# Kernel tuning notes

Hardware: AMD Instinct MI355X
Metric: run time of the kernel (lower is better)

## Reference

```python
import jax, jax.numpy as jnp
import numpy as np

B, S, D = 4, 4096, 256


def setup_inputs() -> dict:
    key = jax.random.key(0)
    k1, k2, k3, k4, k5 = jax.random.split(key, 5)
    query = jax.random.normal(k1, (B, S, D), dtype=jnp.float32)
    key_t = jax.random.normal(k2, (B, S, D), dtype=jnp.float32)
    value = jax.random.normal(k3, (B, S, D), dtype=jnp.float32)
    # nn.Linear(dim_model, dim_model): weight [D, D] (out, in), bias [D]
    bound = 1.0 / np.sqrt(D)
    Wq = jax.random.uniform(k4, (D, D), dtype=jnp.float32, minval=-bound, maxval=bound)
    bq = jax.random.uniform(k5, (D,), dtype=jnp.float32, minval=-bound, maxval=bound)
    return {"query": query, "key": key_t, "value": value, "Wq": Wq, "bq": bq}


def reference(query, key, value, Wq, bq):
    # Faithful to source: self.q is applied to ALL THREE inputs (source bug).
    q = jnp.einsum('bsd,od->bso', query, Wq) + bq  # [B,S,D]
    k = jnp.einsum('bsd,od->bso', key, Wq) + bq
    v = jnp.einsum('bsd,od->bso', value, Wq) + bq
    scale = jnp.sqrt(jnp.asarray(q.shape[-1], q.dtype))
    scores = jnp.einsum('bqd,bkd->bqk', q, k) / scale  # [B,S,S]
    attn = jax.nn.softmax(scores, axis=-1)
    return jnp.einsum('bqk,bkd->bqd', attn, v)  # [B,S,D]
```

## Files before the change

kernel.cpp:

```cpp
#include <hip/hip_runtime.h>


typedef __attribute__((ext_vector_type(4)))  float    f32x4;
typedef __attribute__((ext_vector_type(16))) float    f32x16;
typedef __attribute__((ext_vector_type(8)))  short    s16x8;
typedef __attribute__((ext_vector_type(2)))  unsigned u32x2;

#define AS_GLB const __attribute__((address_space(1))) unsigned
#define AS_LDS __attribute__((address_space(3))) unsigned

static constexpr float CEXP = 0.09016844f;
static constexpr float CM   = -32.0f * 0.09016844f;

static constexpr size_t QBF_OFF = 0;
static constexpr size_t KBF_OFF = 8ull  << 20;
static constexpr size_t VTB_OFF = 16ull << 20;
static constexpr size_t OT_OFF  = 24ull << 20;
static constexpr size_t LS_OFF  = 56ull << 20;

__device__ __forceinline__ unsigned bf16_rne(float f) {
  union { float f; unsigned u; } v; v.f = f;
  return (v.u + 0x7FFFu + ((v.u >> 16) & 1u)) >> 16;
}
__device__ __forceinline__ unsigned pkbf16(float a, float b) {
  return bf16_rne(a) | (bf16_rne(b) << 16);
}

__global__ __launch_bounds__(256, 2) void proj_kernel(
    const float* __restrict__ Xq, const float* __restrict__ Xk,
    const float* __restrict__ Xv, const float* __restrict__ Wq,
    const float* __restrict__ bq, char* __restrict__ ws)
{
  __shared__ char plds[32768];
  const int tid = threadIdx.x;
  const int lane = tid & 63, w = tid >> 6;
  const int wr = w >> 1, wc = w & 1;
  const int l15 = lane & 15, l4 = (lane >> 4) & 3;

  const int mt = blockIdx.x;
  const int tensor = mt >> 7;
  const int r0 = (mt & 127) << 7;
  const int n0 = blockIdx.y << 7;
  const float* A = (tensor == 0) ? Xq : (tensor == 1 ? Xk : Xv);

  f32x4 acc[4][4];
#pragma unroll
  for (int i = 0; i < 4; ++i)
#pragma unroll
    for (int j = 0; j < 4; ++j) { acc[i][j][0]=0.f; acc[i][j][1]=0.f; acc[i][j][2]=0.f; acc[i][j][3]=0.f; }

  for (int kt = 0; kt < 4; ++kt) {
    const int k0 = kt << 6;
#pragma unroll
    for (int j = 0; j < 8; ++j) {
      int c = j * 256 + tid;
      int row = c >> 4, col4 = c & 15;
      f32x4 av = *(const f32x4*)(A + (size_t)(r0 + row) * 256 + k0 + col4 * 4);
      u32x2 pa; pa[0] = pkbf16(av[0], av[1]); pa[1] = pkbf16(av[2], av[3]);
      int off = row * 128 + ((col4 * 8) ^ ((row & 7) << 4));
      *(u32x2*)(plds + off) = pa;
      f32x4 wv = *(const f32x4*)(Wq + (size_t)(n0 + row) * 256 + k0 + col4 * 4);
      u32x2 pw; pw[0] = pkbf16(wv[0], wv[1]); pw[1] = pkbf16(wv[2], wv[3]);
      *(u32x2*)(plds + 16384 + off) = pw;
    }
    __syncthreads();
#pragma unroll
    for (int ks = 0; ks < 2; ++ks) {
      s16x8 af[4], wf[4];
#pragma unroll
      for (int mi = 0; mi < 4; ++mi) {
        int row = wr * 64 + mi * 16 + l15;
        af[mi] = *(const s16x8*)(plds + row * 128 + ((ks * 64 + l4 * 16) ^ ((row & 7) << 4)));
      }
#pragma unroll
      for (int ni = 0; ni < 4; ++ni) {
        int row = wc * 64 + ni * 16 + l15;
        wf[ni] = *(const s16x8*)(plds + 16384 + row * 128 + ((ks * 64 + l4 * 16) ^ ((row & 7) << 4)));
      }
      if (tensor == 1) {
#pragma unroll
        for (int mi = 0; mi < 4; ++mi)
#pragma unroll
          for (int ni = 0; ni < 4; ++ni)
            acc[mi][ni] = __builtin_amdgcn_mfma_f32_16x16x32_bf16(wf[ni], af[mi], acc[mi][ni], 0, 0, 0);
      } else {
#pragma unroll
        for (int mi = 0; mi < 4; ++mi)
#pragma unroll
          for (int ni = 0; ni < 4; ++ni)
            acc[mi][ni] = __builtin_amdgcn_mfma_f32_16x16x32_bf16(af[mi], wf[ni], acc[mi][ni], 0, 0, 0);
      }
    }
    __syncthreads();
  }

  if (tensor == 0) {
    unsigned short* Qb = (unsigned short*)(ws + QBF_OFF);
#pragma unroll
    for (int ni = 0; ni < 4; ++ni) {
      int gn = n0 + wc * 64 + ni * 16 + l15;
      float bias = bq[gn];
#pragma unroll
      for (int mi = 0; mi < 4; ++mi) {
        int mrow = r0 + wr * 64 + mi * 16 + l4 * 4;
#pragma unroll
        for (int j = 0; j < 4; ++j)
          Qb[(size_t)(mrow + j) * 256 + gn] = (unsigned short)bf16_rne(acc[mi][ni][j] + bias);
      }
    }
  } else if (tensor == 1) {
    char* Kf = ws + KBF_OFF;
#pragma unroll
    for (int ni = 0; ni < 4; ++ni) {
      int dbase = n0 + wc * 64 + ni * 16 + l4 * 4;
      f32x4 bv = *(const f32x4*)(bq + dbase);
#pragma unroll
      for (int mi = 0; mi < 4; ++mi) {
        int s = r0 + wr * 64 + mi * 16 + l15;
        int b2 = s >> 12, sl = s & 31, kb = (s & 4095) >> 5;
        size_t chunk = (((size_t)b2 * 128 + kb) * 32 + (dbase >> 3)) * 32 + sl;
        u32x2 pv;
        pv[0] = pkbf16(acc[mi][ni][0] + bv[0], acc[mi][ni][1] + bv[1]);
        pv[1] = pkbf16(acc[mi][ni][2] + bv[2], acc[mi][ni][3] + bv[3]);
        *(u32x2*)(Kf + chunk * 16 + (dbase & 7) * 2) = pv;
      }
    }
  } else {
    char* Vf = ws + VTB_OFF;
#pragma unroll
    for (int ni = 0; ni < 4; ++ni) {
      int gn = n0 + wc * 64 + ni * 16 + l15;
      float bias = bq[gn];
#pragma unroll
      for (int mi = 0; mi < 4; ++mi) {
        int s = r0 + wr * 64 + mi * 16 + l4 * 4;
        int b2 = s >> 12, kb = (s & 4095) >> 5, sl = s & 31;
        size_t chunk = ((((size_t)b2 * 128 + kb) * 4 + (sl >> 3)) * 8 + (gn >> 5)) * 32 + (gn & 31);
        u32x2 pv;
        pv[0] = pkbf16(acc[mi][ni][0] + bias, acc[mi][ni][1] + bias);
        pv[1] = pkbf16(acc[mi][ni][2] + bias, acc[mi][ni][3] + bias);
        *(u32x2*)(Vf + chunk * 16 + (sl & 7) * 2) = pv;
      }
    }
  }
}

__global__ __launch_bounds__(256, 2) void flash_kernel(char* __restrict__ ws)
{
  __shared__ char lds[65536];
  const int tid = threadIdx.x;
  const int lane = tid & 63, w = tid >> 6;
  const int l31 = lane & 31, h = lane >> 5;

  const int bid  = blockIdx.x;
  const int sp   = bid & 3;
  const int b    = (bid >> 2) & 3;
  const int qblk = bid >> 4;
  const int q0w  = qblk * 128 + w * 32;
  const int kb0  = sp * 32;

  const char* Kfb = ws + KBF_OFF + (size_t)b * (2u << 20);
  const char* Vfb = ws + VTB_OFF + (size_t)b * (2u << 20);

  s16x8 qf[16];
  {
    const char* qrow = ws + QBF_OFF + (size_t)((b << 12) + q0w + l31) * 512 + h * 16;
#pragma unroll
    for (int i = 0; i < 16; ++i) qf[i] = *(const s16x8*)(qrow + i * 32);
  }
#pragma unroll
  for (int i = 0; i < 16; ++i) asm volatile("" :: "v"(qf[i]));

  f32x16 O[8];
#pragma unroll
  for (int t8 = 0; t8 < 8; ++t8)
#pragma unroll
    for (int r = 0; r < 16; ++r) O[t8][r] = 0.f;

  float l_run = 0.f;

  auto STAGE = [&](int buf, int t) {
    const char* ksrc = Kfb + (size_t)(kb0 + t) * 16384;
    const char* vsrc = Vfb + (size_t)(kb0 + t) * 16384;
#pragma unroll
    for (int i = 0; i < 4; ++i) {
      unsigned c = (unsigned)(w * 4 + i) << 10;
      __builtin_amdgcn_global_load_lds((AS_GLB*)(ksrc + c + (unsigned)lane * 16),
          (AS_LDS*)(lds + buf * 32768 + c), 16, 0, 0);
      __builtin_amdgcn_global_load_lds((AS_GLB*)(vsrc + c + (unsigned)lane * 16),
          (AS_LDS*)(lds + buf * 32768 + 16384 + c), 16, 0, 0);
    }
  };

  auto COMPUTE = [&](int buf) {
    const char* kb = lds + buf * 32768;
    const char* vb = kb + 16384;
    f32x16 pe, po;
#pragma unroll
    for (int r = 0; r < 16; ++r) { pe[r] = 0.f; po[r] = 0.f; }
    __builtin_amdgcn_s_setprio(1);
#pragma unroll
    for (int i = 0; i < 16; i += 2) {
      s16x8 kf0 = *(const s16x8*)(kb + (2 * i + h) * 512 + l31 * 16);
      pe = __builtin_amdgcn_mfma_f32_32x32x16_bf16(kf0, qf[i], pe, 0, 0, 0);
      s16x8 kf1 = *(const s16x8*)(kb + (2 * (i + 1) + h) * 512 + l31 * 16);
      po = __builtin_amdgcn_mfma_f32_32x32x16_bf16(kf1, qf[i + 1], po, 0, 0, 0);
    }
    __builtin_amdgcn_s_setprio(0);
    float p[16];
#pragma unroll
    for (int r = 0; r < 16; ++r)
      p[r] = __builtin_exp2f(__builtin_fmaf(pe[r] + po[r], CEXP, CM));
    float s0 = (p[0] + p[1]) + (p[2] + p[3]);
    float s1 = (p[4] + p[5]) + (p[6] + p[7]);
    float s2 = (p[8] + p[9]) + (p[10] + p[11]);
    float s3 = (p[12] + p[13]) + (p[14] + p[15]);
    l_run += (s0 + s1) + (s2 + s3);
    unsigned a0, a1, b0, b1, c0, c1, d0, d1;
    asm("v_cvt_pk_bf16_f32 %0, %1, %2" : "=v"(a0) : "v"(p[0]),  "v"(p[1]));
    asm("v_cvt_pk_bf16_f32 %0, %1, %2" : "=v"(a1) : "v"(p[2]),  "v"(p[3]));
    asm("v_cvt_pk_bf16_f32 %0, %1, %2" : "=v"(b0) : "v"(p[4]),  "v"(p[5]));
    asm("v_cvt_pk_bf16_f32 %0, %1, %2" : "=v"(b1) : "v"(p[6]),  "v"(p[7]));
    asm("v_cvt_pk_bf16_f32 %0, %1, %2" : "=v"(c0) : "v"(p[8]),  "v"(p[9]));
    asm("v_cvt_pk_bf16_f32 %0, %1, %2" : "=v"(c1) : "v"(p[10]), "v"(p[11]));
    asm("v_cvt_pk_bf16_f32 %0, %1, %2" : "=v"(d0) : "v"(p[12]), "v"(p[13]));
    asm("v_cvt_pk_bf16_f32 %0, %1, %2" : "=v"(d1) : "v"(p[14]), "v"(p[15]));
    asm("v_permlane32_swap_b32 %0, %1" : "+v"(a0), "+v"(b0));
    asm("v_permlane32_swap_b32 %0, %1" : "+v"(a1), "+v"(b1));
    asm("v_permlane32_swap_b32 %0, %1" : "+v"(c0), "+v"(d0));
    asm("v_permlane32_swap_b32 %0, %1" : "+v"(c1), "+v"(d1));
    union { s16x8 v; unsigned u[4]; } pa0, pa1;
    pa0.u[0] = a0; pa0.u[1] = a1; pa0.u[2] = b0; pa0.u[3] = b1;
    pa1.u[0] = c0; pa1.u[1] = c1; pa1.u[2] = d0; pa1.u[3] = d1;
    __builtin_amdgcn_s_setprio(1);
#pragma unroll
    for (int t8 = 0; t8 < 8; ++t8) {
      s16x8 v0 = *(const s16x8*)(vb + ((h * 8 + t8) << 9) + l31 * 16);
      O[t8] = __builtin_amdgcn_mfma_f32_32x32x16_bf16(pa0.v, v0, O[t8], 0, 0, 0);
      s16x8 v1 = *(const s16x8*)(vb + (((2 + h) * 8 + t8) << 9) + l31 * 16);
      O[t8] = __builtin_amdgcn_mfma_f32_32x32x16_bf16(pa1.v, v1, O[t8], 0, 0, 0);
    }
    __builtin_amdgcn_s_setprio(0);
  };

  STAGE(0, 0);
  for (int t = 0; t < 31; ++t) {
    STAGE((t + 1) & 1, t + 1);
    asm volatile("s_waitcnt vmcnt(8)" ::: "memory");
    __builtin_amdgcn_s_barrier();
    __builtin_amdgcn_sched_barrier(0);
    COMPUTE(t & 1);
    __builtin_amdgcn_s_barrier();
    __builtin_amdgcn_sched_barrier(0);
  }
  asm volatile("s_waitcnt vmcnt(0)" ::: "memory");
  __builtin_amdgcn_s_barrier();
  __builtin_amdgcn_sched_barrier(0);
  COMPUTE(1);

  l_run += __shfl_xor(l_run, 32, 64);

  unsigned short* OTb = (unsigned short*)(ws + OT_OFF) +
                        (((size_t)(sp * 4 + b) << 12) << 8);
#pragma unroll
  for (int t8 = 0; t8 < 8; ++t8) {
    int d = t8 * 32 + l31;
#pragma unroll
    for (int r = 0; r < 16; ++r) {
      int q = q0w + (r & 3) + 8 * (r >> 2) + 4 * h;
      OTb[(size_t)q * 256 + d] = (unsigned short)bf16_rne(O[t8][r]);
    }
  }
  if (lane < 32) {
    int idx = ((sp * 4 + b) << 12) + q0w + l31;
    ((float*)(ws + LS_OFF))[idx] = l_run;
  }
}

__global__ __launch_bounds__(256) void merge_kernel(const char* __restrict__ ws,
                                                    float* __restrict__ out)
{
  const int t = threadIdx.x;
  const int b = blockIdx.x;
  const int s0 = blockIdx.y << 4;
  const int soff = t >> 7, dd = (t & 127) * 2;
  const unsigned short* OTb = (const unsigned short*)(ws + OT_OFF);
  const float* Ls = (const float*)(ws + LS_OFF);
  for (int si = 0; si < 8; ++si) {
    int s = s0 + si * 2 + soff;
    float L = 0.f;
#pragma unroll
    for (int sp = 0; sp < 4; ++sp) L += Ls[((sp * 4 + b) << 12) + s];
    float rL = 1.0f / L;
    float a0 = 0.f, a1 = 0.f;
#pragma unroll
    for (int sp = 0; sp < 4; ++sp) {
      unsigned uv = *(const unsigned*)(OTb + ((((size_t)(sp * 4 + b) << 12) + s) << 8) + dd);
      union { unsigned u; float f; } lo, hi;
      lo.u = uv << 16; hi.u = uv & 0xFFFF0000u;
      a0 += lo.f; a1 += hi.f;
    }
    float2 o; o.x = a0 * rL; o.y = a1 * rL;
    *(float2*)(out + (((size_t)(b << 12) + s) << 8) + dd) = o;
  }
}

extern "C" void kernel_launch(void* const* d_in, const int* in_sizes, int n_in,
                              void* d_out, int out_size, void* d_ws, size_t ws_size,
                              hipStream_t stream) {
  const float* q  = (const float*)d_in[0];
  const float* k  = (const float*)d_in[1];
  const float* v  = (const float*)d_in[2];
  const float* Wq = (const float*)d_in[3];
  const float* bq = (const float*)d_in[4];
  char* ws = (char*)d_ws;
  float* out = (float*)d_out;
  hipLaunchKernelGGL(proj_kernel, dim3(384, 2), dim3(256), 0, stream, q, k, v, Wq, bq, ws);
  hipLaunchKernelGGL(flash_kernel, dim3(512), dim3(256), 0, stream, ws);
  hipLaunchKernelGGL(merge_kernel, dim3(4, 256), dim3(256), 0, stream, ws, out);
}
```

Measured before the change: 112.3 us.

## Software-pipeline QK and PV across iterations with split K/V staging

Restructures the attention loop so the PV matmul of the previous tile is issued after the QK matmul of the current tile, letting the exp/convert work of one tile overlap the MFMA work of another. K and V now use separate double buffers with separate staging, and V is loaded one iteration later than K. The two interleaved QK accumulators become a single one, which lengthens the dependent MFMA chain. The probabilities are carried across iterations in registers, which raises register pressure.

New measurement: 110.7 us. No clear change (-1.4%).

```diff
diff --git a/kernel.cpp b/kernel.cpp
--- a/kernel.cpp
+++ b/kernel.cpp
@@ -178,39 +178,65 @@
     for (int r = 0; r < 16; ++r) O[t8][r] = 0.f;
 
   float l_run = 0.f;
-
-  auto STAGE = [&](int buf, int t) {
+  s16x8 paP0, paP1;
+
+  auto STAGE_K = [&](int buf, int t) {
     const char* ksrc = Kfb + (size_t)(kb0 + t) * 16384;
-    const char* vsrc = Vfb + (size_t)(kb0 + t) * 16384;
 #pragma unroll
     for (int i = 0; i < 4; ++i) {
       unsigned c = (unsigned)(w * 4 + i) << 10;
       __builtin_amdgcn_global_load_lds((AS_GLB*)(ksrc + c + (unsigned)lane * 16),
-          (AS_LDS*)(lds + buf * 32768 + c), 16, 0, 0);
+          (AS_LDS*)(lds + buf * 16384 + c), 16, 0, 0);
+    }
+  };
+  auto STAGE_V = [&](int buf, int t) {
+    const char* vsrc = Vfb + (size_t)(kb0 + t) * 16384;
+#pragma unroll
+    for (int i = 0; i < 4; ++i) {
+      unsigned c = (unsigned)(w * 4 + i) << 10;
       __builtin_amdgcn_global_load_lds((AS_GLB*)(vsrc + c + (unsigned)lane * 16),
-          (AS_LDS*)(lds + buf * 32768 + 16384 + c), 16, 0, 0);
+          (AS_LDS*)(lds + 32768 + buf * 16384 + c), 16, 0, 0);
     }
   };
-
-  auto COMPUTE = [&](int buf) {
-    const char* kb = lds + buf * 32768;
-    const char* vb = kb + 16384;
-    f32x16 pe, po;
-#pragma unroll
-    for (int r = 0; r < 16; ++r) { pe[r] = 0.f; po[r] = 0.f; }
+  auto PV = [&](const char* vb, s16x8 a0, s16x8 a1) {
     __builtin_amdgcn_s_setprio(1);
 #pragma unroll
-    for (int i = 0; i < 16; i += 2) {
-      s16x8 kf0 = *(const s16x8*)(kb + (2 * i + h) * 512 + l31 * 16);
-      pe = __builtin_amdgcn_mfma_f32_32x32x16_bf16(kf0, qf[i], pe, 0, 0, 0);
-      s16x8 kf1 = *(const s16x8*)(kb + (2 * (i + 1) + h) * 512 + l31 * 16);
-      po = __builtin_amdgcn_mfma_f32_32x32x16_bf16(kf1, qf[i + 1], po, 0, 0, 0);
+    for (int t8 = 0; t8 < 8; ++t8) {
+      s16x8 v0 = *(const s16x8*)(vb + ((h * 8 + t8) << 9) + l31 * 16);
+      O[t8] = __builtin_amdgcn_mfma_f32_32x32x16_bf16(a0, v0, O[t8], 0, 0, 0);
+      s16x8 v1 = *(const s16x8*)(vb + (((2 + h) * 8 + t8) << 9) + l31 * 16);
+      O[t8] = __builtin_amdgcn_mfma_f32_32x32x16_bf16(a1, v1, O[t8], 0, 0, 0);
     }
     __builtin_amdgcn_s_setprio(0);
+  };
+
+  STAGE_K(0, 0);
+  for (int t = 0; t < 32; ++t) {
+    if (t + 1 < 32) STAGE_K((t + 1) & 1, t + 1);
+    STAGE_V(t & 1, t);
+    if (t + 1 < 32) { asm volatile("s_waitcnt vmcnt(8)" ::: "memory"); }
+    else            { asm volatile("s_waitcnt vmcnt(4)" ::: "memory"); }
+    __builtin_amdgcn_s_barrier();
+    __builtin_amdgcn_sched_barrier(0);
+
+    const char* kb = lds + (t & 1) * 16384;
+    f32x16 pacc;
+#pragma unroll
+    for (int r = 0; r < 16; ++r) pacc[r] = 0.f;
+    __builtin_amdgcn_s_setprio(1);
+#pragma unroll
+    for (int i = 0; i < 16; ++i) {
+      s16x8 kf = *(const s16x8*)(kb + ((2 * i + h) << 9) + l31 * 16);
+      pacc = __builtin_amdgcn_mfma_f32_32x32x16_bf16(kf, qf[i], pacc, 0, 0, 0);
+    }
+    __builtin_amdgcn_s_setprio(0);
+
+    if (t > 0) PV(lds + 32768 + ((t - 1) & 1) * 16384, paP0, paP1);
+
     float p[16];
 #pragma unroll
     for (int r = 0; r < 16; ++r)
-      p[r] = __builtin_exp2f(__builtin_fmaf(pe[r] + po[r], CEXP, CM));
+      p[r] = __builtin_exp2f(__builtin_fmaf(pacc[r], CEXP, CM));
     float s0 = (p[0] + p[1]) + (p[2] + p[3]);
     float s1 = (p[4] + p[5]) + (p[6] + p[7]);
     float s2 = (p[8] + p[9]) + (p[10] + p[11]);
@@ -229,34 +255,18 @@
     asm("v_permlane32_swap_b32 %0, %1" : "+v"(a1), "+v"(b1));
     asm("v_permlane32_swap_b32 %0, %1" : "+v"(c0), "+v"(d0));
     asm("v_permlane32_swap_b32 %0, %1" : "+v"(c1), "+v"(d1));
-    union { s16x8 v; unsigned u[4]; } pa0, pa1;
-    pa0.u[0] = a0; pa0.u[1] = a1; pa0.u[2] = b0; pa0.u[3] = b1;
-    pa1.u[0] = c0; pa1.u[1] = c1; pa1.u[2] = d0; pa1.u[3] = d1;
-    __builtin_amdgcn_s_setprio(1);
-#pragma unroll
-    for (int t8 = 0; t8 < 8; ++t8) {
-      s16x8 v0 = *(const s16x8*)(vb + ((h * 8 + t8) << 9) + l31 * 16);
-      O[t8] = __builtin_amdgcn_mfma_f32_32x32x16_bf16(pa0.v, v0, O[t8], 0, 0, 0);
-      s16x8 v1 = *(const s16x8*)(vb + (((2 + h) * 8 + t8) << 9) + l31 * 16);
-      O[t8] = __builtin_amdgcn_mfma_f32_32x32x16_bf16(pa1.v, v1, O[t8], 0, 0, 0);
-    }
-    __builtin_amdgcn_s_setprio(0);
-  };
-
-  STAGE(0, 0);
-  for (int t = 0; t < 31; ++t) {
-    STAGE((t + 1) & 1, t + 1);
-    asm volatile("s_waitcnt vmcnt(8)" ::: "memory");
-    __builtin_amdgcn_s_barrier();
-    __builtin_amdgcn_sched_barrier(0);
-    COMPUTE(t & 1);
+    union { s16x8 v; unsigned u[4]; } u0, u1;
+    u0.u[0] = a0; u0.u[1] = a1; u0.u[2] = b0; u0.u[3] = b1;
+    u1.u[0] = c0; u1.u[1] = c1; u1.u[2] = d0; u1.u[3] = d1;
+    paP0 = u0.v; paP1 = u1.v;
+
     __builtin_amdgcn_s_barrier();
     __builtin_amdgcn_sched_barrier(0);
   }
   asm volatile("s_waitcnt vmcnt(0)" ::: "memory");
   __builtin_amdgcn_s_barrier();
   __builtin_amdgcn_sched_barrier(0);
-  COMPUTE(1);
+  PV(lds + 32768 + 16384, paP0, paP1);
 
   l_run += __shfl_xor(l_run, 32, 64);
 
```

## Fuse split-KV merge into flash kernel via last-arriver atomic counter

Applied to the files above, without the earlier changes.

Adds per-(batch, query-block) atomic counters, zeroed in the projection kernel, so the last of the four split-KV flash blocks to finish performs the merge of partial outputs and normalizers directly. This removes the separate merge kernel launch and its scheduling gap. The merge work then runs on only a quarter of the blocks, serialized at the tail of each group, and it relies on threadfence ordering. The fused path is chosen only when the workspace is large enough, otherwise the old merge kernel is used.

Result: slower. 220.8 us (+96.7%).

```diff
diff --git a/kernel.cpp b/kernel.cpp
--- a/kernel.cpp
+++ b/kernel.cpp
@@ -17,6 +17,8 @@
 static constexpr size_t VTB_OFF = 16ull << 20;
 static constexpr size_t OT_OFF  = 24ull << 20;
 static constexpr size_t LS_OFF  = 56ull << 20;
+static constexpr size_t CNT_OFF = LS_OFF + (256ull << 10);
+static constexpr size_t WS_NEEDED = CNT_OFF + 512;
 
 __device__ __forceinline__ unsigned bf16_rne(float f) {
   union { float f; unsigned u; } v; v.f = f;
@@ -43,6 +45,9 @@
   const int n0 = blockIdx.y << 7;
   const float* A = (tensor == 0) ? Xq : (tensor == 1 ? Xk : Xv);
 
+  if (mt == 0 && blockIdx.y == 0 && tid < 128)
+    ((int*)(ws + CNT_OFF))[tid] = 0;
+
   f32x4 acc[4][4];
 #pragma unroll
   for (int i = 0; i < 4; ++i)
@@ -145,7 +150,9 @@
   }
 }
 
-__global__ __launch_bounds__(256, 2) void flash_kernel(char* __restrict__ ws)
+__global__ __launch_bounds__(256, 2) void flash_kernel(char* __restrict__ ws,
+                                                       float* __restrict__ out,
+                                                       int fuse)
 {
   __shared__ char lds[65536];
   const int tid = threadIdx.x;
@@ -275,6 +282,51 @@
     int idx = ((sp * 4 + b) << 12) + q0w + l31;
     ((float*)(ws + LS_OFF))[idx] = l_run;
   }
+
+  if (!fuse) return;
+
+  __syncthreads();
+  __threadfence();
+  if (tid == 0) {
+    int old = atomicAdd((int*)(ws + CNT_OFF) + ((b << 5) | qblk), 1);
+    ((int*)lds)[0] = old;
+  }
+  __syncthreads();
+  if (((int*)lds)[0] == 3) {
+    __threadfence();
+    const int q0 = qblk * 128;
+    const unsigned short* OTall = (const unsigned short*)(ws + OT_OFF);
+    const float* Ls = (const float*)(ws + LS_OFF);
+    const int r = tid >> 1;
+    const int dh = (tid & 1) * 128;
+    const int q = q0 + r;
+    float L = 0.f;
+#pragma unroll
+    for (int s2 = 0; s2 < 4; ++s2) L += Ls[((s2 * 4 + b) << 12) + q];
+    const float rL = 1.0f / L;
+    float* op = out + ((size_t)((b << 12) + q)) * 256 + dh;
+#pragma unroll
+    for (int d0 = 0; d0 < 16; ++d0) {
+      float acc8[8];
+#pragma unroll
+      for (int j = 0; j < 8; ++j) acc8[j] = 0.f;
+#pragma unroll
+      for (int s2 = 0; s2 < 4; ++s2) {
+        s16x8 vv = *(const s16x8*)(OTall + ((((size_t)(s2 * 4 + b) << 12) + q) << 8) + dh + d0 * 8);
+#pragma unroll
+        for (int j = 0; j < 8; ++j) {
+          union { unsigned u; float f; } cv;
+          cv.u = ((unsigned)(unsigned short)vv[j]) << 16;
+          acc8[j] += cv.f;
+        }
+      }
+      f32x4 o0, o1;
+#pragma unroll
+      for (int j = 0; j < 4; ++j) { o0[j] = acc8[j] * rL; o1[j] = acc8[4 + j] * rL; }
+      *(f32x4*)(op + d0 * 8) = o0;
+      *(f32x4*)(op + d0 * 8 + 4) = o1;
+    }
+  }
 }
 
 __global__ __launch_bounds__(256) void merge_kernel(const char* __restrict__ ws,
@@ -315,7 +367,9 @@
   const float* bq = (const float*)d_in[4];
   char* ws = (char*)d_ws;
   float* out = (float*)d_out;
+  const int fuse = (ws_size >= WS_NEEDED) ? 1 : 0;
   hipLaunchKernelGGL(proj_kernel, dim3(384, 2), dim3(256), 0, stream, q, k, v, Wq, bq, ws);
-  hipLaunchKernelGGL(flash_kernel, dim3(512), dim3(256), 0, stream, ws);
-  hipLaunchKernelGGL(merge_kernel, dim3(4, 256), dim3(256), 0, stream, ws, out);
-}
+  hipLaunchKernelGGL(flash_kernel, dim3(512), dim3(256), 0, stream, ws, out, fuse);
+  if (!fuse)
+    hipLaunchKernelGGL(merge_kernel, dim3(4, 256), dim3(256), 0, stream, ws, out);
+}
```
